# Kernel optimization log

Measured on AMD Instinct MI355X. Metric: run time of the kernel, lower is better.

Reference implementation:

```python
import jax, jax.numpy as jnp
import numpy as np

B, S, D = 4, 256, 768      # batch, seq, activation_dim
F = 8192                   # dict_size (both modules)
K = 64                     # topk
C = 128                    # connections per downstream feature


def _topk_keep(post, k):
    """Keep top-k entries per row, zero elsewhere. post: [N, F]."""
    vals, idx = jax.lax.top_k(post, k)
    n = post.shape[0]
    return jnp.zeros_like(post).at[jnp.arange(n)[:, None], idx].set(vals)


def setup_inputs() -> dict:
    key = jax.random.key(0)
    ks = jax.random.split(key, 10)
    s = 1.0 / np.sqrt(D)
    return {
        "initial_acts": jax.random.normal(ks[0], (B, S, D), jnp.float32),
        "x_up": jax.random.normal(ks[1], (B, S, D), jnp.float32),
        "ln_scale": jax.random.uniform(ks[2], (B, S), jnp.float32, 0.5, 1.5),
        "W_enc_up": jax.random.normal(ks[3], (F, D), jnp.float32) * s,
        "b_enc_up": jnp.zeros((F,), jnp.float32),
        "W_dec_up": jax.random.normal(ks[4], (D, F), jnp.float32) * s,
        "b_dec_up": jax.random.normal(ks[5], (D,), jnp.float32) * 0.01,
        "W_enc_down": jax.random.normal(ks[6], (F, D), jnp.float32) * s,
        "b_enc_down": jnp.zeros((F,), jnp.float32),
        "W_dec_down": jax.random.normal(ks[7], (D, F), jnp.float32) * s,
        "b_dec_down": jax.random.normal(ks[8], (D,), jnp.float32) * 0.01,
        "conn": jax.random.randint(ks[9], (F, C), 0, F),  # all valid (no -1 pad)
    }


def reference(initial_acts, x_up, ln_scale,
              W_enc_up, b_enc_up, W_dec_up, b_dec_up,
              W_enc_down, b_enc_down, W_dec_down, b_dec_down,
              conn):
    b, s, d = initial_acts.shape
    n = b * s
    x0 = initial_acts.reshape(n, d)
    xu = x_up.reshape(n, d)
    ln = ln_scale.reshape(n)

    # --- vanilla_forward on upstream: TopK SAE encode + decode ---
    post_up = jax.nn.relu((xu - b_dec_up) @ W_enc_up.T + b_enc_up)  # [n, F]
    feat_up = _topk_keep(post_up, K)
    recon_up = feat_up @ W_dec_up.T + b_dec_up                      # [n, d]

    # --- pruned downstream path ---
    fd = W_enc_down.shape[0]
    fu = W_dec_up.shape[1]
    # virtual weights: down_encoder @ up_decoder  -> [F_down, F_up]
    virtual = W_enc_down @ W_dec_up
    # connection mask from index tensor [F_down, C]
    mask = jnp.zeros((fd, fu), bool).at[jnp.arange(fd)[:, None], conn].set(True)
    masked = jnp.where(mask, virtual, jnp.zeros((), virtual.dtype))

    approx = x0 @ W_enc_down.T                                      # initial contributions [n, F_down]
    approx = approx + feat_up @ masked.T + W_enc_down @ b_dec_up    # pruned contributions + b_dec term
    approx = approx / ln[:, None] + b_enc_down - W_enc_down @ b_dec_down

    feat_down = _topk_keep(approx, K)
    recon_down = feat_down @ W_dec_down.T + b_dec_down              # [n, d]

    return jnp.stack([recon_up.reshape(b, s, d), recon_down.reshape(b, s, d)])
```

## Files before the change

kernel.cpp:

```cpp
#include <hip/hip_runtime.h>


#define NTOK 1024
#define DIM  768
#define FF   8192
#define KK   64
#define CC   128
#define KSEL_UP 80
#define KSEL_DN 96
#define CAP  128

typedef unsigned short u16;
typedef unsigned int   u32;
typedef __attribute__((ext_vector_type(8))) short short8;
typedef __attribute__((ext_vector_type(4))) float floatx4;

__device__ __forceinline__ float bits2f(u32 v) {
    float f; __builtin_memcpy(&f, &v, 4); return f;
}
__device__ __forceinline__ float bf2f(u16 u) { return bits2f(((u32)u) << 16); }
__device__ __forceinline__ u16 f2bf(float f) {
    u32 u; __builtin_memcpy(&u, &f, 4);
    u32 lsb = (u >> 16) & 1u;
    u += 0x7fffu + lsb;
    return (u16)(u >> 16);
}
__device__ __forceinline__ u16 bfkey(u16 b) {
    return (b & 0x8000u) ? (u16)~b : (u16)(b | 0x8000u);
}

__global__ __launch_bounds__(256) void convert_kernel(const float* __restrict__ src,
                                                      u16* __restrict__ dst, int n4) {
    int i = blockIdx.x * 256 + threadIdx.x;
    if (i < n4) {
        float4 v = ((const float4*)src)[i];
        ushort4 o;
        o.x = f2bf(v.x); o.y = f2bf(v.y); o.z = f2bf(v.z); o.w = f2bf(v.w);
        ((ushort4*)dst)[i] = o;
    }
}

__global__ __launch_bounds__(256) void transpose_kernel(const float* __restrict__ in,
                                                        float* __restrict__ out) {
    __shared__ float tile[32][33];
    int f0 = blockIdx.x * 32, d0 = blockIdx.y * 32;
    int tx = threadIdx.x, ty = threadIdx.y;
#pragma unroll
    for (int i = 0; i < 4; ++i)
        tile[ty + 8 * i][tx] = in[(size_t)(d0 + ty + 8 * i) * FF + f0 + tx];
    __syncthreads();
#pragma unroll
    for (int i = 0; i < 4; ++i)
        out[(size_t)(f0 + ty + 8 * i) * DIM + d0 + tx] = tile[tx][ty + 8 * i];
}

__global__ __launch_bounds__(256) void transpose16_kernel(const float* __restrict__ in,
                                                          u16* __restrict__ out) {
    __shared__ float tile[32][33];
    int f0 = blockIdx.x * 32, d0 = blockIdx.y * 32;
    int tx = threadIdx.x, ty = threadIdx.y;
#pragma unroll
    for (int i = 0; i < 4; ++i)
        tile[ty + 8 * i][tx] = in[(size_t)(d0 + ty + 8 * i) * FF + f0 + tx];
    __syncthreads();
#pragma unroll
    for (int i = 0; i < 4; ++i)
        out[(size_t)(f0 + ty + 8 * i) * DIM + d0 + tx] = f2bf(tile[tx][ty + 8 * i]);
}

__global__ __launch_bounds__(64) void bias_kernel(const float* __restrict__ Weu,
                                                  const float* __restrict__ Wed,
                                                  const float* __restrict__ bdu,
                                                  const float* __restrict__ bdd,
                                                  const float* __restrict__ bed,
                                                  float* __restrict__ sF,
                                                  float* __restrict__ tuF,
                                                  float* __restrict__ c2F,
                                                  double* __restrict__ s64,
                                                  double* __restrict__ tu64,
                                                  double* __restrict__ td64) {
    int f = blockIdx.x, lane = threadIdx.x;
    double su = 0.0, tu = 0.0, td = 0.0;
    for (int i = lane; i < DIM; i += 64) {
        double bu = (double)bdu[i], bd = (double)bdd[i];
        su += (double)Weu[(size_t)f * DIM + i] * bu;
        double w = (double)Wed[(size_t)f * DIM + i];
        tu += w * bu;
        td += w * bd;
    }
#pragma unroll
    for (int off = 32; off; off >>= 1) {
        su += __shfl_xor(su, off);
        tu += __shfl_xor(tu, off);
        td += __shfl_xor(td, off);
    }
    if (lane == 0) {
        sF[f] = (float)su; tuF[f] = (float)tu;
        c2F[f] = (float)((double)bed[f] - td);
        s64[f] = su; tu64[f] = tu; td64[f] = td;
    }
}

template <int MODE>
__global__ __launch_bounds__(256) void gemm_mfma(const u16* __restrict__ A16,
                                                 const u16* __restrict__ B16,
                                                 u16* __restrict__ Xout,
                                                 const float* __restrict__ sF,
                                                 const float* __restrict__ b_enc) {
    __shared__ __align__(16) u16 As[128 * 40];
    __shared__ __align__(16) u16 Bs[128 * 40];
    int tid = threadIdx.x;
    int wave = tid >> 6, lane = tid & 63;
    int lm = lane & 15, quad = lane >> 4;
    int m0 = blockIdx.y * 128, n0 = blockIdx.x * 128;
    int wm = (wave >> 1) * 64, wn = (wave & 1) * 64;
    floatx4 acc[4][4];
#pragma unroll
    for (int i = 0; i < 4; ++i)
#pragma unroll
        for (int j = 0; j < 4; ++j)
            acc[i][j] = (floatx4){0.f, 0.f, 0.f, 0.f};
    int r = tid >> 2;
    int s = (tid & 3) * 8;
    const u16* gA = A16 + (size_t)(m0 + r) * DIM + s;
    const u16* gB = B16 + (size_t)(n0 + r) * DIM + s;
    for (int k0 = 0; k0 < DIM; k0 += 32) {
        __syncthreads();
        *(int4*)&As[r * 40 + s]          = *(const int4*)(gA + k0);
        *(int4*)&As[(r + 64) * 40 + s]   = *(const int4*)(gA + (size_t)64 * DIM + k0);
        *(int4*)&Bs[r * 40 + s]          = *(const int4*)(gB + k0);
        *(int4*)&Bs[(r + 64) * 40 + s]   = *(const int4*)(gB + (size_t)64 * DIM + k0);
        __syncthreads();
        short8 af[4], bfr[4];
#pragma unroll
        for (int mi = 0; mi < 4; ++mi)
            af[mi] = *(const short8*)&As[(wm + mi * 16 + lm) * 40 + quad * 8];
#pragma unroll
        for (int ni = 0; ni < 4; ++ni)
            bfr[ni] = *(const short8*)&Bs[(wn + ni * 16 + lm) * 40 + quad * 8];
#pragma unroll
        for (int mi = 0; mi < 4; ++mi)
#pragma unroll
            for (int ni = 0; ni < 4; ++ni)
                acc[mi][ni] = __builtin_amdgcn_mfma_f32_16x16x32_bf16(
                    af[mi], bfr[ni], acc[mi][ni], 0, 0, 0);
    }
#pragma unroll
    for (int ni = 0; ni < 4; ++ni) {
        int col = n0 + wn + ni * 16 + lm;
        float sub = 0.f, bb = 0.f;
        if (MODE == 0) { sub = sF[col]; bb = b_enc[col]; }
#pragma unroll
        for (int mi = 0; mi < 4; ++mi) {
#pragma unroll
            for (int reg = 0; reg < 4; ++reg) {
                int row = m0 + wm + mi * 16 + quad * 4 + reg;
                float v = acc[mi][ni][reg];
                if (MODE == 0) { v = v - sub + bb; v = v > 0.f ? v : 0.f; }
                Xout[(size_t)row * FF + col] = f2bf(v);
            }
        }
    }
}

__device__ void find_threshold(u32* hist, int k, u32* sc) {
    int tid = threadIdx.x;
    for (int st = 1; st < 256; st <<= 1) {
        u32 v = 0;
        if (tid < 256) {
            v = hist[tid];
            if (tid + st < 256) v += hist[tid + st];
        }
        __syncthreads();
        if (tid < 256) hist[tid] = v;
        __syncthreads();
    }
    if (tid < 256) {
        u32 ge = hist[tid];
        u32 gn = (tid < 255) ? hist[tid + 1] : 0u;
        if ((int)ge >= k && (int)gn < k) { sc[0] = (u32)tid; sc[1] = (u32)(k - (int)gn); }
    }
    __syncthreads();
}

template <typename KT>
__device__ void radix_collect(const KT* __restrict__ keys, u32* hist, int* eqidx,
                              u32* sc, int ksel, u16* cr, int* cnt_out, int row) {
    int tid = threadIdx.x;
    if (tid < 256) hist[tid] = 0;
    __syncthreads();
    for (int i = tid; i < FF; i += 256) atomicAdd(&hist[((u32)keys[i] & 0xffffu) >> 8], 1u);
    __syncthreads();
    find_threshold(hist, ksel, sc);
    int hb = (int)sc[0], k1 = (int)sc[1];
    if (tid < 256) hist[tid] = 0;
    __syncthreads();
    for (int i = tid; i < FF; i += 256) {
        u32 k = (u32)keys[i] & 0xffffu;
        if ((int)(k >> 8) == hb) atomicAdd(&hist[k & 255u], 1u);
    }
    __syncthreads();
    find_threshold(hist, k1, sc);
    u32 T = ((u32)hb << 8) | sc[0];
    if (tid == 0) { sc[2] = 0; sc[3] = 0; }
    __syncthreads();
    for (int i = tid; i < FF; i += 256) {
        u32 k = (u32)keys[i] & 0xffffu;
        if (k > T) {
            u32 p = atomicAdd(&sc[2], 1u);
            if (p < CAP) cr[p] = (u16)i;
        } else if (k == T) {
            u32 p = atomicAdd(&sc[3], 1u);
            if (p < 256) eqidx[p] = i;
        }
    }
    __syncthreads();
    if (tid == 0) {
        int G = (int)sc[2]; if (G > CAP) G = CAP;
        int ne = (int)sc[3]; if (ne > 256) ne = 256;
        int total = G;
        for (int q = 0; q < ne && total < CAP; ++q) cr[total++] = (u16)eqidx[q];
        cnt_out[row] = total;
    }
}

__global__ __launch_bounds__(256) void select_up_kernel(const u16* __restrict__ X16,
                                                        u16* __restrict__ cand,
                                                        int* __restrict__ cnt) {
    __shared__ u16 keys[FF];
    __shared__ u32 hist[256];
    __shared__ int eqidx[256];
    __shared__ u32 sc[4];
    const int row = blockIdx.x, tid = threadIdx.x;
    const ushort4* src = (const ushort4*)(X16 + (size_t)row * FF);
    for (int i = tid; i < FF / 4; i += 256) {
        ushort4 u = src[i];
        keys[i * 4]     = bfkey(u.x);
        keys[i * 4 + 1] = bfkey(u.y);
        keys[i * 4 + 2] = bfkey(u.z);
        keys[i * 4 + 3] = bfkey(u.w);
    }
    __syncthreads();
    radix_collect<u16>(keys, hist, eqidx, sc, KSEL_UP, cand + (size_t)row * CAP, cnt, row);
}

__device__ __forceinline__ bool sort_before(double av, int ai, double bv, int bi) {
    return (av > bv) || (av == bv && ai < bi);
}
__device__ void bitonic128(double* sv, int* si, int tid) {
    for (int k = 2; k <= 128; k <<= 1) {
        for (int j = k >> 1; j > 0; j >>= 1) {
            __syncthreads();
            if (tid < 64) {
                int i = ((tid & ~(j - 1)) << 1) | (tid & (j - 1));
                int l = i, rr = i + j;
                bool bfirst = sort_before(sv[rr], si[rr], sv[l], si[l]);
                bool doswap = ((i & k) == 0) ? bfirst : !bfirst;
                if (doswap) {
                    double tv = sv[l]; sv[l] = sv[rr]; sv[rr] = tv;
                    int ti = si[l]; si[l] = si[rr]; si[rr] = ti;
                }
            }
        }
    }
    __syncthreads();
}

__global__ __launch_bounds__(512) void fixup_up(const float* __restrict__ xu,
                                                const float* __restrict__ Weu,
                                                const double* __restrict__ s64,
                                                const float* __restrict__ beu,
                                                const u16* __restrict__ cand,
                                                const int* __restrict__ cnt,
                                                float* __restrict__ vals,
                                                int* __restrict__ idxs) {
    __shared__ float xrow[DIM];
    __shared__ double sv[128];
    __shared__ int si[128];
    int t = blockIdx.x, tid = threadIdx.x, wave = tid >> 6, lane = tid & 63;
    for (int i = tid; i < DIM; i += 512) xrow[i] = xu[(size_t)t * DIM + i];
    for (int c = tid; c < 128; c += 512) { sv[c] = -1.0e300; si[c] = 0x7fffffff; }
    __syncthreads();
    int nc = cnt[t]; if (nc > 128) nc = 128;
    for (int c = wave; c < nc; c += 8) {
        int f = (int)cand[(size_t)t * CAP + c];
        const float* wr = Weu + (size_t)f * DIM;
        double p = 0.0;
#pragma unroll
        for (int i = 0; i < 12; ++i) {
            int d = lane + 64 * i;
            p += (double)xrow[d] * (double)wr[d];
        }
#pragma unroll
        for (int off = 32; off; off >>= 1) p += __shfl_xor(p, off);
        if (lane == 0) {
            double v = p - s64[f] + (double)beu[f];
            v = v > 0.0 ? v : 0.0;
            sv[c] = v; si[c] = f;
        }
    }
    __syncthreads();
    bitonic128(sv, si, tid);
    if (tid < KK) {
        vals[(size_t)t * KK + tid] = (float)sv[tid];
        idxs[(size_t)t * KK + tid] = si[tid];
    }
}

__global__ __launch_bounds__(512) void fixup_dn(const float* __restrict__ x0,
                                                const float* __restrict__ Wed,
                                                const float* __restrict__ WduT,
                                                const double* __restrict__ tu64,
                                                const double* __restrict__ td64,
                                                const float* __restrict__ bed,
                                                const float* __restrict__ ln,
                                                const u16* __restrict__ cclean,
                                                const float* __restrict__ vals_up,
                                                const int* __restrict__ idx_up,
                                                const u16* __restrict__ cand,
                                                const int* __restrict__ cnt,
                                                float* __restrict__ vals,
                                                int* __restrict__ idxs) {
    __shared__ float xrow[DIM];
    __shared__ u32 bm[256];
    __shared__ int fl[KK];
    __shared__ float zl[KK];
    __shared__ double sv[128];
    __shared__ int si[128];
    int t = blockIdx.x, tid = threadIdx.x, wave = tid >> 6, lane = tid & 63;
    for (int i = tid; i < DIM; i += 512) xrow[i] = x0[(size_t)t * DIM + i];
    if (tid < 256) bm[tid] = 0;
    for (int c = tid; c < 128; c += 512) { sv[c] = -1.0e300; si[c] = 0x7fffffff; }
    __syncthreads();
    if (tid < KK) {
        int f = idx_up[(size_t)t * KK + tid];
        fl[tid] = f; zl[tid] = vals_up[(size_t)t * KK + tid];
        atomicOr(&bm[f >> 5], 1u << (f & 31));
    }
    __syncthreads();
    int nc = cnt[t]; if (nc > 128) nc = 128;
    double lnt = (double)ln[t];
    for (int c = wave; c < nc; c += 8) {
        int f = (int)cand[(size_t)t * CAP + c];
        const float* wr = Wed + (size_t)f * DIM;
        double p = 0.0;
#pragma unroll
        for (int i = 0; i < 12; ++i) {
            int d = lane + 64 * i;
            p += (double)xrow[d] * (double)wr[d];
        }
        const u16* crow = cclean + (size_t)f * CC;
        int e0 = (int)crow[lane], e1 = (int)crow[lane + 64];
        bool h0 = (e0 != 0xFFFF) && ((bm[e0 >> 5] >> (e0 & 31)) & 1u);
        bool h1 = (e1 != 0xFFFF) && ((bm[e1 >> 5] >> (e1 & 31)) & 1u);
        unsigned long long m0 = __ballot(h0), m1 = __ballot(h1);
        while (m0 | m1) {
            int fu;
            if (m0) {
                int b = __ffsll((long long)m0) - 1; m0 &= m0 - 1;
                fu = __shfl(e0, b);
            } else {
                int b = __ffsll((long long)m1) - 1; m1 &= m1 - 1;
                fu = __shfl(e1, b);
            }
            unsigned long long zm = __ballot(fl[lane] == fu);
            float z = zl[__ffsll((long long)zm) - 1];
            const float* du = WduT + (size_t)fu * DIM;
            double vp = 0.0;
#pragma unroll
            for (int i = 0; i < 12; ++i) {
                int d = lane + 64 * i;
                vp += (double)wr[d] * (double)du[d];
            }
            p += (double)z * vp;
        }
#pragma unroll
        for (int off = 32; off; off >>= 1) p += __shfl_xor(p, off);
        if (lane == 0) {
            double v = (p + tu64[f]) / lnt + (double)bed[f] - td64[f];
            sv[c] = v; si[c] = f;
        }
    }
    __syncthreads();
    bitonic128(sv, si, tid);
    if (tid < KK) {
        vals[(size_t)t * KK + tid] = (float)sv[tid];
        idxs[(size_t)t * KK + tid] = si[tid];
    }
}

__global__ __launch_bounds__(128) void dedup_deg_kernel(const int* __restrict__ conn,
                                                        u32* __restrict__ deg) {
    __shared__ int row[CC];
    int fd = blockIdx.x, c = threadIdx.x;
    int v = conn[(size_t)fd * CC + c];
    row[c] = v;
    __syncthreads();
    bool dup = false;
    for (int j = 0; j < c; ++j) dup |= (row[j] == v);
    if (!dup) atomicAdd(&deg[v], 1u);
}

__global__ __launch_bounds__(256) void scan_kernel(const u32* __restrict__ deg,
                                                   u32* __restrict__ offs) {
    __shared__ u32 sdeg[FF];
    __shared__ u32 part[256];
    int tid = threadIdx.x;
    for (int i = tid; i < FF; i += 256) sdeg[i] = deg[i];
    __syncthreads();
    u32 s = 0;
    for (int j = 0; j < 32; ++j) s += sdeg[tid * 32 + j];
    part[tid] = s;
    __syncthreads();
    if (tid == 0) {
        u32 run = 0;
        for (int i = 0; i < 256; ++i) { u32 v = part[i]; part[i] = run; run += v; }
        offs[FF] = run;
    }
    __syncthreads();
    u32 run = part[tid];
    for (int j = 0; j < 32; ++j) { offs[tid * 32 + j] = run; run += sdeg[tid * 32 + j]; }
}

__global__ __launch_bounds__(128) void fill_kernel(const int* __restrict__ conn,
                                                   const u32* __restrict__ offs,
                                                   u32* __restrict__ cursor,
                                                   u16* __restrict__ inv_fd,
                                                   u16* __restrict__ cclean) {
    __shared__ int row[CC];
    int fd = blockIdx.x, c = threadIdx.x;
    int v = conn[(size_t)fd * CC + c];
    row[c] = v;
    __syncthreads();
    bool dup = false;
    for (int j = 0; j < c; ++j) dup |= (row[j] == v);
    cclean[(size_t)fd * CC + c] = dup ? (u16)0xFFFF : (u16)v;
    if (!dup) {
        u32 slot = atomicAdd(&cursor[v], 1u);
        inv_fd[offs[v] + slot] = (u16)fd;
    }
}

__global__ __launch_bounds__(256) void vconn_chunk(const u16* __restrict__ Wed16,
                                                   const float* __restrict__ WduT,
                                                   const u32* __restrict__ offs,
                                                   const u16* __restrict__ inv_fd,
                                                   u32* __restrict__ pe,
                                                   int chunk, int first) {
    __shared__ float row[192];
    int fu = blockIdx.x, tid = threadIdx.x;
    if (tid < 192) row[tid] = WduT[(size_t)fu * DIM + chunk * 192 + tid];
    __syncthreads();
    u32 s = offs[fu], e = offs[fu + 1];
    int wave = tid >> 6, lane = tid & 63;
    int sub = lane >> 4, sl = lane & 15;
    for (u32 p0 = s + (u32)wave * 4; p0 < e; p0 += 16) {
        u32 p = p0 + (u32)sub;
        bool valid = p < e;
        float a = 0.f;
        int fd = 0;
        u32 old = 0;
        if (valid) {
            if (first) fd = (int)inv_fd[p];
            else { old = pe[p]; fd = (int)(old >> 16); }
            const u16* wr = Wed16 + (size_t)fd * DIM + chunk * 192;
#pragma unroll
            for (int i = 0; i < 12; ++i)
                a = fmaf(bf2f(wr[sl + 16 * i]), row[sl + 16 * i], a);
        }
        a += __shfl_xor(a, 1);
        a += __shfl_xor(a, 2);
        a += __shfl_xor(a, 4);
        a += __shfl_xor(a, 8);
        if (valid && sl == 0) {
            float v = first ? a : (bf2f((u16)(old & 0xffffu)) + a);
            pe[p] = ((u32)fd << 16) | (u32)f2bf(v);
        }
    }
}

__global__ __launch_bounds__(256) void phase2sel(const u16* __restrict__ X16,
                                                 const float* __restrict__ vals_up,
                                                 const int* __restrict__ idx_up,
                                                 const u32* __restrict__ offs,
                                                 const u32* __restrict__ pe,
                                                 const float* __restrict__ tuF,
                                                 const float* __restrict__ c2F,
                                                 const float* __restrict__ ln,
                                                 u16* __restrict__ cand,
                                                 int* __restrict__ cnt) {
    __shared__ u32 accbits[FF];
    __shared__ float zl[KK];
    __shared__ u32 offs_s[KK];
    __shared__ u32 ends_s[KK];
    __shared__ u32 hist[256];
    __shared__ int eqidx[256];
    __shared__ u32 sc[4];
    float* facc = (float*)accbits;
    int t = blockIdx.x, tid = threadIdx.x, wave = tid >> 6, lane = tid & 63;
    for (int i = tid; i < FF; i += 256) accbits[i] = 0u;
    if (tid < KK) {
        int f = idx_up[(size_t)t * KK + tid];
        zl[tid] = vals_up[(size_t)t * KK + tid];
        offs_s[tid] = offs[f];
        ends_s[tid] = offs[f + 1];
    }
    __syncthreads();
    for (int j = wave; j < KK; j += 4) {
        u32 s = offs_s[j], e = ends_s[j];
        float zj = zl[j];
        u32 p = s + (u32)lane;
        u32 v0 = 0, v1 = 0, v2 = 0;
        bool h0 = p < e, h1 = p + 64 < e, h2 = p + 128 < e;
        if (h0) v0 = pe[p];
        if (h1) v1 = pe[p + 64];
        if (h2) v2 = pe[p + 128];
        if (h0) atomicAdd(&facc[v0 >> 16], zj * bf2f((u16)(v0 & 0xffffu)));
        if (h1) atomicAdd(&facc[v1 >> 16], zj * bf2f((u16)(v1 & 0xffffu)));
        if (h2) atomicAdd(&facc[v2 >> 16], zj * bf2f((u16)(v2 & 0xffffu)));
        for (u32 q = p + 192; q < e; q += 64) {
            u32 v = pe[q];
            atomicAdd(&facc[v >> 16], zj * bf2f((u16)(v & 0xffffu)));
        }
    }
    __syncthreads();
    float lnv = ln[t];
    const ushort4* xs = (const ushort4*)(X16 + (size_t)t * FF);
    const float4* tu4 = (const float4*)tuF;
    const float4* c24 = (const float4*)c2F;
    for (int i = tid; i < FF / 4; i += 256) {
        ushort4 u = xs[i];
        float4 tu = tu4[i], c2 = c24[i];
        int i4 = i * 4;
        float a0 = facc[i4], a1 = facc[i4 + 1], a2 = facc[i4 + 2], a3 = facc[i4 + 3];
        accbits[i4]     = (u32)bfkey(f2bf((bf2f(u.x) + a0 + tu.x) / lnv + c2.x));
        accbits[i4 + 1] = (u32)bfkey(f2bf((bf2f(u.y) + a1 + tu.y) / lnv + c2.y));
        accbits[i4 + 2] = (u32)bfkey(f2bf((bf2f(u.z) + a2 + tu.z) / lnv + c2.z));
        accbits[i4 + 3] = (u32)bfkey(f2bf((bf2f(u.w) + a3 + tu.w) / lnv + c2.w));
    }
    __syncthreads();
    radix_collect<u32>(accbits, hist, eqidx, sc, KSEL_DN, cand + (size_t)t * CAP, cnt, t);
}

__global__ __launch_bounds__(256) void decode_both(const float* __restrict__ vals_up,
                                                   const int* __restrict__ idx_up,
                                                   const float* __restrict__ vals_dn,
                                                   const int* __restrict__ idx_dn,
                                                   const u16* __restrict__ WduT16,
                                                   const u16* __restrict__ WddT16,
                                                   const float* __restrict__ bdu,
                                                   const float* __restrict__ bdd,
                                                   float* __restrict__ outp) {
    __shared__ float z[KK];
    __shared__ int fidx[KK];
    int b = blockIdx.x, tid = threadIdx.x;
    int which = b >> 10, t = b & 1023;
    const float* vals = which ? vals_dn : vals_up;
    const int* idxs = which ? idx_dn : idx_up;
    const u16* WdT = which ? WddT16 : WduT16;
    const float* bd = which ? bdd : bdu;
    float* o = outp + (size_t)which * NTOK * DIM + (size_t)t * DIM;
    if (tid < KK) { z[tid] = vals[(size_t)t * KK + tid]; fidx[tid] = idxs[(size_t)t * KK + tid]; }
    __syncthreads();
    float a0 = 0.f, a1 = 0.f, a2 = 0.f;
    for (int j = 0; j < KK; ++j) {
        const u16* wr = WdT + (size_t)fidx[j] * DIM;
        float zj = z[j];
        a0 = fmaf(zj, bf2f(wr[tid]), a0);
        a1 = fmaf(zj, bf2f(wr[tid + 256]), a1);
        a2 = fmaf(zj, bf2f(wr[tid + 512]), a2);
    }
    o[tid]       = a0 + bd[tid];
    o[tid + 256] = a1 + bd[tid + 256];
    o[tid + 512] = a2 + bd[tid + 512];
}

extern "C" void kernel_launch(void* const* d_in, const int* in_sizes, int n_in,
                              void* d_out, int out_size, void* d_ws, size_t ws_size,
                              hipStream_t stream) {
    const float* x0  = (const float*)d_in[0];
    const float* xu  = (const float*)d_in[1];
    const float* ln  = (const float*)d_in[2];
    const float* Weu = (const float*)d_in[3];
    const float* beu = (const float*)d_in[4];
    const float* Wdu = (const float*)d_in[5];
    const float* bdu = (const float*)d_in[6];
    const float* Wed = (const float*)d_in[7];
    const float* bed = (const float*)d_in[8];
    const float* Wdd = (const float*)d_in[9];
    const float* bdd = (const float*)d_in[10];
    const int* conn = (const int*)d_in[11];
    float* out = (float*)d_out;

    char* w = (char*)d_ws;
    size_t off = 0;
    auto take = [&](size_t bytes) { char* p = w + off; off = (off + bytes + 255) & ~(size_t)255; return p; };
    u16*   X16     = (u16*)take((size_t)NTOK * FF * 2);
    u16*   B16     = (u16*)take((size_t)FF * DIM * 2);
    u16*   WddT16  = X16;
    u16*   WduT16  = B16;
    float* WduT    = (float*)take((size_t)FF * DIM * 4);
    u16*   A16     = (u16*)take((size_t)NTOK * DIM * 2);
    u16*   inv_fd  = (u16*)take((size_t)FF * CC * 2);
    u16*   cclean  = (u16*)take((size_t)FF * CC * 2);
    u32*   pe      = (u32*)take((size_t)FF * CC * 4);
    u16*   cand_u  = (u16*)take((size_t)NTOK * CAP * 2);
    u16*   cand_d  = (u16*)take((size_t)NTOK * CAP * 2);
    int*   cnt_u   = (int*)take(NTOK * 4);
    int*   cnt_d   = (int*)take(NTOK * 4);
    float* vals_up = (float*)take((size_t)NTOK * KK * 4);
    int*   idx_up  = (int*)take((size_t)NTOK * KK * 4);
    float* vals_dn = (float*)take((size_t)NTOK * KK * 4);
    int*   idx_dn  = (int*)take((size_t)NTOK * KK * 4);
    float* sF      = (float*)take(FF * 4);
    float* tuF     = (float*)take(FF * 4);
    float* c2F     = (float*)take(FF * 4);
    double* s64    = (double*)take(FF * 8);
    double* tu64   = (double*)take(FF * 8);
    double* td64   = (double*)take(FF * 8);
    u32*   deg     = (u32*)take(FF * 4);
    u32*   cursor  = (u32*)take(FF * 4);
    u32*   offs    = (u32*)take((FF + 8) * 4);

    dim3 tgrid(FF / 32, DIM / 32), tblk(32, 8);
    dim3 ggrid(FF / 128, NTOK / 128);
    int nA4 = NTOK * DIM / 4, nB4 = FF * DIM / 4;

    transpose_kernel<<<tgrid, tblk, 0, stream>>>(Wdu, WduT);
    bias_kernel<<<FF, 64, 0, stream>>>(Weu, Wed, bdu, bdd, bed, sF, tuF, c2F,
                                       s64, tu64, td64);
    hipMemsetAsync(deg, 0, 2 * FF * sizeof(u32), stream);
    dedup_deg_kernel<<<FF, CC, 0, stream>>>(conn, deg);
    scan_kernel<<<1, 256, 0, stream>>>(deg, offs);
    fill_kernel<<<FF, CC, 0, stream>>>(conn, offs, cursor, inv_fd, cclean);

    convert_kernel<<<(nA4 + 255) / 256, 256, 0, stream>>>(xu, A16, nA4);
    convert_kernel<<<(nB4 + 255) / 256, 256, 0, stream>>>(Weu, B16, nB4);
    gemm_mfma<0><<<ggrid, 256, 0, stream>>>(A16, B16, X16, sF, beu);
    select_up_kernel<<<NTOK, 256, 0, stream>>>(X16, cand_u, cnt_u);
    fixup_up<<<NTOK, 512, 0, stream>>>(xu, Weu, s64, beu, cand_u, cnt_u, vals_up, idx_up);

    convert_kernel<<<(nA4 + 255) / 256, 256, 0, stream>>>(x0, A16, nA4);
    convert_kernel<<<(nB4 + 255) / 256, 256, 0, stream>>>(Wed, B16, nB4);
    gemm_mfma<1><<<ggrid, 256, 0, stream>>>(A16, B16, X16, sF, beu);
    vconn_chunk<<<FF, 256, 0, stream>>>(B16, WduT, offs, inv_fd, pe, 0, 1);
    vconn_chunk<<<FF, 256, 0, stream>>>(B16, WduT, offs, inv_fd, pe, 1, 0);
    vconn_chunk<<<FF, 256, 0, stream>>>(B16, WduT, offs, inv_fd, pe, 2, 0);
    vconn_chunk<<<FF, 256, 0, stream>>>(B16, WduT, offs, inv_fd, pe, 3, 0);
    convert_kernel<<<(nB4 + 255) / 256, 256, 0, stream>>>(WduT, WduT16, nB4);
    phase2sel<<<NTOK, 256, 0, stream>>>(X16, vals_up, idx_up, offs, pe,
                                        tuF, c2F, ln, cand_d, cnt_d);
    fixup_dn<<<NTOK, 512, 0, stream>>>(x0, Wed, WduT, tu64, td64, bed, ln, cclean,
                                       vals_up, idx_up, cand_d, cnt_d, vals_dn, idx_dn);

    transpose16_kernel<<<tgrid, tblk, 0, stream>>>(Wdd, WddT16);
    decode_both<<<2 * NTOK, 256, 0, stream>>>(vals_up, idx_up, vals_dn, idx_dn,
                                              WduT16, WddT16, bdu, bdd, out);
}
```

Measured before the change: 781.4 us.

## Fuse fp32-to-bf16 conversion into GEMM loads, widen select kernels, vectorize fixups

The encoder GEMM now reads fp32 activations and weights directly and packs them to bf16 while staging into shared memory, which removes three separate convert launches and their intermediate buffers. The selection kernels (select_up, phase2sel) run with 512 threads instead of 256, and the fixup dot products use float4 loads. The downstream candidate count drops from 96 to 80. In exchange the GEMM moves twice the global bytes per tile, and the smaller candidate margin could hurt exact top-k correctness if bf16 ranking errors are larger than expected.

```diff
diff --git a/kernel.cpp b/kernel.cpp
--- a/kernel.cpp
+++ b/kernel.cpp
@@ -7,7 +7,7 @@
 #define KK   64
 #define CC   128
 #define KSEL_UP 80
-#define KSEL_DN 96
+#define KSEL_DN 80
 #define CAP  128
 
 typedef unsigned short u16;
@@ -27,6 +27,14 @@
 }
 __device__ __forceinline__ u16 bfkey(u16 b) {
     return (b & 0x8000u) ? (u16)~b : (u16)(b | 0x8000u);
+}
+__device__ __forceinline__ int4 pack8(float4 a, float4 b) {
+    int4 r;
+    r.x = (int)((u32)f2bf(a.x) | ((u32)f2bf(a.y) << 16));
+    r.y = (int)((u32)f2bf(a.z) | ((u32)f2bf(a.w) << 16));
+    r.z = (int)((u32)f2bf(b.x) | ((u32)f2bf(b.y) << 16));
+    r.w = (int)((u32)f2bf(b.z) | ((u32)f2bf(b.w) << 16));
+    return r;
 }
 
 __global__ __launch_bounds__(256) void convert_kernel(const float* __restrict__ src,
@@ -102,8 +110,8 @@
 }
 
 template <int MODE>
-__global__ __launch_bounds__(256) void gemm_mfma(const u16* __restrict__ A16,
-                                                 const u16* __restrict__ B16,
+__global__ __launch_bounds__(256) void gemm_mfma(const float* __restrict__ Af,
+                                                 const float* __restrict__ Bf,
                                                  u16* __restrict__ Xout,
                                                  const float* __restrict__ sF,
                                                  const float* __restrict__ b_enc) {
@@ -122,14 +130,22 @@
             acc[i][j] = (floatx4){0.f, 0.f, 0.f, 0.f};
     int r = tid >> 2;
     int s = (tid & 3) * 8;
-    const u16* gA = A16 + (size_t)(m0 + r) * DIM + s;
-    const u16* gB = B16 + (size_t)(n0 + r) * DIM + s;
+    const float* gA = Af + (size_t)(m0 + r) * DIM + s;
+    const float* gB = Bf + (size_t)(n0 + r) * DIM + s;
     for (int k0 = 0; k0 < DIM; k0 += 32) {
+        float4 a0 = *(const float4*)(gA + k0);
+        float4 a1 = *(const float4*)(gA + k0 + 4);
+        float4 a2 = *(const float4*)(gA + (size_t)64 * DIM + k0);
+        float4 a3 = *(const float4*)(gA + (size_t)64 * DIM + k0 + 4);
+        float4 b0 = *(const float4*)(gB + k0);
+        float4 b1 = *(const float4*)(gB + k0 + 4);
+        float4 b2 = *(const float4*)(gB + (size_t)64 * DIM + k0);
+        float4 b3 = *(const float4*)(gB + (size_t)64 * DIM + k0 + 4);
         __syncthreads();
-        *(int4*)&As[r * 40 + s]          = *(const int4*)(gA + k0);
-        *(int4*)&As[(r + 64) * 40 + s]   = *(const int4*)(gA + (size_t)64 * DIM + k0);
-        *(int4*)&Bs[r * 40 + s]          = *(const int4*)(gB + k0);
-        *(int4*)&Bs[(r + 64) * 40 + s]   = *(const int4*)(gB + (size_t)64 * DIM + k0);
+        *(int4*)&As[r * 40 + s]        = pack8(a0, a1);
+        *(int4*)&As[(r + 64) * 40 + s] = pack8(a2, a3);
+        *(int4*)&Bs[r * 40 + s]        = pack8(b0, b1);
+        *(int4*)&Bs[(r + 64) * 40 + s] = pack8(b2, b3);
         __syncthreads();
         short8 af[4], bfr[4];
 #pragma unroll
@@ -186,16 +202,16 @@
 template <typename KT>
 __device__ void radix_collect(const KT* __restrict__ keys, u32* hist, int* eqidx,
                               u32* sc, int ksel, u16* cr, int* cnt_out, int row) {
-    int tid = threadIdx.x;
+    int tid = threadIdx.x, bs = blockDim.x;
     if (tid < 256) hist[tid] = 0;
     __syncthreads();
-    for (int i = tid; i < FF; i += 256) atomicAdd(&hist[((u32)keys[i] & 0xffffu) >> 8], 1u);
+    for (int i = tid; i < FF; i += bs) atomicAdd(&hist[((u32)keys[i] & 0xffffu) >> 8], 1u);
     __syncthreads();
     find_threshold(hist, ksel, sc);
     int hb = (int)sc[0], k1 = (int)sc[1];
     if (tid < 256) hist[tid] = 0;
     __syncthreads();
-    for (int i = tid; i < FF; i += 256) {
+    for (int i = tid; i < FF; i += bs) {
         u32 k = (u32)keys[i] & 0xffffu;
         if ((int)(k >> 8) == hb) atomicAdd(&hist[k & 255u], 1u);
     }
@@ -204,7 +220,7 @@
     u32 T = ((u32)hb << 8) | sc[0];
     if (tid == 0) { sc[2] = 0; sc[3] = 0; }
     __syncthreads();
-    for (int i = tid; i < FF; i += 256) {
+    for (int i = tid; i < FF; i += bs) {
         u32 k = (u32)keys[i] & 0xffffu;
         if (k > T) {
             u32 p = atomicAdd(&sc[2], 1u);
@@ -224,7 +240,7 @@
     }
 }
 
-__global__ __launch_bounds__(256) void select_up_kernel(const u16* __restrict__ X16,
+__global__ __launch_bounds__(512) void select_up_kernel(const u16* __restrict__ X16,
                                                         u16* __restrict__ cand,
                                                         int* __restrict__ cnt) {
     __shared__ u16 keys[FF];
@@ -233,7 +249,7 @@
     __shared__ u32 sc[4];
     const int row = blockIdx.x, tid = threadIdx.x;
     const ushort4* src = (const ushort4*)(X16 + (size_t)row * FF);
-    for (int i = tid; i < FF / 4; i += 256) {
+    for (int i = tid; i < FF / 4; i += 512) {
         ushort4 u = src[i];
         keys[i * 4]     = bfkey(u.x);
         keys[i * 4 + 1] = bfkey(u.y);
@@ -282,15 +298,18 @@
     for (int c = tid; c < 128; c += 512) { sv[c] = -1.0e300; si[c] = 0x7fffffff; }
     __syncthreads();
     int nc = cnt[t]; if (nc > 128) nc = 128;
+    const float4* xr4 = (const float4*)xrow;
     for (int c = wave; c < nc; c += 8) {
         int f = (int)cand[(size_t)t * CAP + c];
-        const float* wr = Weu + (size_t)f * DIM;
-        double p = 0.0;
-#pragma unroll
-        for (int i = 0; i < 12; ++i) {
-            int d = lane + 64 * i;
-            p += (double)xrow[d] * (double)wr[d];
-        }
+        const float4* wr4 = (const float4*)(Weu + (size_t)f * DIM);
+        float4 w0 = wr4[lane], w1 = wr4[lane + 64], w2 = wr4[lane + 128];
+        float4 x0 = xr4[lane], x1 = xr4[lane + 64], x2 = xr4[lane + 128];
+        double p = (double)x0.x * w0.x + (double)x0.y * w0.y
+                 + (double)x0.z * w0.z + (double)x0.w * w0.w;
+        p += (double)x1.x * w1.x + (double)x1.y * w1.y
+           + (double)x1.z * w1.z + (double)x1.w * w1.w;
+        p += (double)x2.x * w2.x + (double)x2.y * w2.y
+           + (double)x2.z * w2.z + (double)x2.w * w2.w;
 #pragma unroll
         for (int off = 32; off; off >>= 1) p += __shfl_xor(p, off);
         if (lane == 0) {
@@ -307,7 +326,7 @@
     }
 }
 
-__global__ __launch_bounds__(512) void fixup_dn(const float* __restrict__ x0,
+__global__ __launch_bounds__(512) void fixup_dn(const float* __restrict__ x0g,
                                                 const float* __restrict__ Wed,
                                                 const float* __restrict__ WduT,
                                                 const double* __restrict__ tu64,
@@ -328,7 +347,7 @@
     __shared__ double sv[128];
     __shared__ int si[128];
     int t = blockIdx.x, tid = threadIdx.x, wave = tid >> 6, lane = tid & 63;
-    for (int i = tid; i < DIM; i += 512) xrow[i] = x0[(size_t)t * DIM + i];
+    for (int i = tid; i < DIM; i += 512) xrow[i] = x0g[(size_t)t * DIM + i];
     if (tid < 256) bm[tid] = 0;
     for (int c = tid; c < 128; c += 512) { sv[c] = -1.0e300; si[c] = 0x7fffffff; }
     __syncthreads();
@@ -340,17 +359,20 @@
     __syncthreads();
     int nc = cnt[t]; if (nc > 128) nc = 128;
     double lnt = (double)ln[t];
+    const float4* xr4 = (const float4*)xrow;
     for (int c = wave; c < nc; c += 8) {
         int f = (int)cand[(size_t)t * CAP + c];
-        const float* wr = Wed + (size_t)f * DIM;
-        double p = 0.0;
-#pragma unroll
-        for (int i = 0; i < 12; ++i) {
-            int d = lane + 64 * i;
-            p += (double)xrow[d] * (double)wr[d];
-        }
+        const float4* wr4 = (const float4*)(Wed + (size_t)f * DIM);
         const u16* crow = cclean + (size_t)f * CC;
         int e0 = (int)crow[lane], e1 = (int)crow[lane + 64];
+        float4 w0 = wr4[lane], w1 = wr4[lane + 64], w2 = wr4[lane + 128];
+        float4 x0 = xr4[lane], x1 = xr4[lane + 64], x2 = xr4[lane + 128];
+        double p = (double)x0.x * w0.x + (double)x0.y * w0.y
+                 + (double)x0.z * w0.z + (double)x0.w * w0.w;
+        p += (double)x1.x * w1.x + (double)x1.y * w1.y
+           + (double)x1.z * w1.z + (double)x1.w * w1.w;
+        p += (double)x2.x * w2.x + (double)x2.y * w2.y
+           + (double)x2.z * w2.z + (double)x2.w * w2.w;
         bool h0 = (e0 != 0xFFFF) && ((bm[e0 >> 5] >> (e0 & 31)) & 1u);
         bool h1 = (e1 != 0xFFFF) && ((bm[e1 >> 5] >> (e1 & 31)) & 1u);
         unsigned long long m0 = __ballot(h0), m1 = __ballot(h1);
@@ -365,13 +387,14 @@
             }
             unsigned long long zm = __ballot(fl[lane] == fu);
             float z = zl[__ffsll((long long)zm) - 1];
-            const float* du = WduT + (size_t)fu * DIM;
-            double vp = 0.0;
-#pragma unroll
-            for (int i = 0; i < 12; ++i) {
-                int d = lane + 64 * i;
-                vp += (double)wr[d] * (double)du[d];
-            }
+            const float4* du4 = (const float4*)(WduT + (size_t)fu * DIM);
+            float4 d0 = du4[lane], d1 = du4[lane + 64], d2 = du4[lane + 128];
+            double vp = (double)w0.x * d0.x + (double)w0.y * d0.y
+                      + (double)w0.z * d0.z + (double)w0.w * d0.w;
+            vp += (double)w1.x * d1.x + (double)w1.y * d1.y
+                + (double)w1.z * d1.z + (double)w1.w * d1.w;
+            vp += (double)w2.x * d2.x + (double)w2.y * d2.y
+                + (double)w2.z * d2.z + (double)w2.w * d2.w;
             p += (double)z * vp;
         }
 #pragma unroll
@@ -479,7 +502,7 @@
     }
 }
 
-__global__ __launch_bounds__(256) void phase2sel(const u16* __restrict__ X16,
+__global__ __launch_bounds__(512) void phase2sel(const u16* __restrict__ X16,
                                                  const float* __restrict__ vals_up,
                                                  const int* __restrict__ idx_up,
                                                  const u32* __restrict__ offs,
@@ -498,7 +521,7 @@
     __shared__ u32 sc[4];
     float* facc = (float*)accbits;
     int t = blockIdx.x, tid = threadIdx.x, wave = tid >> 6, lane = tid & 63;
-    for (int i = tid; i < FF; i += 256) accbits[i] = 0u;
+    for (int i = tid; i < FF; i += 512) accbits[i] = 0u;
     if (tid < KK) {
         int f = idx_up[(size_t)t * KK + tid];
         zl[tid] = vals_up[(size_t)t * KK + tid];
@@ -506,7 +529,7 @@
         ends_s[tid] = offs[f + 1];
     }
     __syncthreads();
-    for (int j = wave; j < KK; j += 4) {
+    for (int j = wave; j < KK; j += 8) {
         u32 s = offs_s[j], e = ends_s[j];
         float zj = zl[j];
         u32 p = s + (u32)lane;
@@ -528,7 +551,7 @@
     const ushort4* xs = (const ushort4*)(X16 + (size_t)t * FF);
     const float4* tu4 = (const float4*)tuF;
     const float4* c24 = (const float4*)c2F;
-    for (int i = tid; i < FF / 4; i += 256) {
+    for (int i = tid; i < FF / 4; i += 512) {
         ushort4 u = xs[i];
         float4 tu = tu4[i], c2 = c24[i];
         int i4 = i * 4;
@@ -600,7 +623,6 @@
     u16*   WddT16  = X16;
     u16*   WduT16  = B16;
     float* WduT    = (float*)take((size_t)FF * DIM * 4);
-    u16*   A16     = (u16*)take((size_t)NTOK * DIM * 2);
     u16*   inv_fd  = (u16*)take((size_t)FF * CC * 2);
     u16*   cclean  = (u16*)take((size_t)FF * CC * 2);
     u32*   pe      = (u32*)take((size_t)FF * CC * 4);
@@ -624,7 +646,7 @@
 
     dim3 tgrid(FF / 32, DIM / 32), tblk(32, 8);
     dim3 ggrid(FF / 128, NTOK / 128);
-    int nA4 = NTOK * DIM / 4, nB4 = FF * DIM / 4;
+    int nB4 = FF * DIM / 4;
 
     transpose_kernel<<<tgrid, tblk, 0, stream>>>(Wdu, WduT);
     bias_kernel<<<FF, 64, 0, stream>>>(Weu, Wed, bdu, bdd, bed, sF, tuF, c2F,
@@ -634,21 +656,18 @@
     scan_kernel<<<1, 256, 0, stream>>>(deg, offs);
     fill_kernel<<<FF, CC, 0, stream>>>(conn, offs, cursor, inv_fd, cclean);
 
-    convert_kernel<<<(nA4 + 255) / 256, 256, 0, stream>>>(xu, A16, nA4);
-    convert_kernel<<<(nB4 + 255) / 256, 256, 0, stream>>>(Weu, B16, nB4);
-    gemm_mfma<0><<<ggrid, 256, 0, stream>>>(A16, B16, X16, sF, beu);
-    select_up_kernel<<<NTOK, 256, 0, stream>>>(X16, cand_u, cnt_u);
+    gemm_mfma<0><<<ggrid, 256, 0, stream>>>(xu, Weu, X16, sF, beu);
+    select_up_kernel<<<NTOK, 512, 0, stream>>>(X16, cand_u, cnt_u);
     fixup_up<<<NTOK, 512, 0, stream>>>(xu, Weu, s64, beu, cand_u, cnt_u, vals_up, idx_up);
 
-    convert_kernel<<<(nA4 + 255) / 256, 256, 0, stream>>>(x0, A16, nA4);
     convert_kernel<<<(nB4 + 255) / 256, 256, 0, stream>>>(Wed, B16, nB4);
-    gemm_mfma<1><<<ggrid, 256, 0, stream>>>(A16, B16, X16, sF, beu);
+    gemm_mfma<1><<<ggrid, 256, 0, stream>>>(x0, Wed, X16, sF, beu);
     vconn_chunk<<<FF, 256, 0, stream>>>(B16, WduT, offs, inv_fd, pe, 0, 1);
     vconn_chunk<<<FF, 256, 0, stream>>>(B16, WduT, offs, inv_fd, pe, 1, 0);
     vconn_chunk<<<FF, 256, 0, stream>>>(B16, WduT, offs, inv_fd, pe, 2, 0);
     vconn_chunk<<<FF, 256, 0, stream>>>(B16, WduT, offs, inv_fd, pe, 3, 0);
     convert_kernel<<<(nB4 + 255) / 256, 256, 0, stream>>>(WduT, WduT16, nB4);
-    phase2sel<<<NTOK, 256, 0, stream>>>(X16, vals_up, idx_up, offs, pe,
+    phase2sel<<<NTOK, 512, 0, stream>>>(X16, vals_up, idx_up, offs, pe,
                                         tuF, c2F, ln, cand_d, cnt_d);
     fixup_dn<<<NTOK, 512, 0, stream>>>(x0, Wed, WduT, tu64, td64, bed, ln, cclean,
                                        vals_up, idx_up, cand_d, cnt_d, vals_dn, idx_dn);
```

After: 774.3 us. No clear change (-0.9%).
